# Kernel optimization log

Measured on AMD Instinct MI355X. Metric: run time of the kernel, lower is better.

## Reference

```python
import jax, jax.numpy as jnp
import numpy as np


def _iir_forward(b_coeff, rho, psi, u_in, y_init, u_init):
    # Coefficient computation: stable 2nd-order resonator parameterization
    r = jax.nn.sigmoid(rho)
    theta = jnp.pi * jax.nn.sigmoid(psi)
    a1 = -2.0 * r * jnp.cos(theta)
    a2 = r * r

    B, T = u_in.shape
    nb = b_coeff.shape[0]  # number of FIR taps (n_b)

    # FIR (moving-average) part, fully vectorized over batch and time:
    # v[t] = sum_k b[k] * u[t-k]; past inputs come from u_init = [u[-1], u[-2], ...]
    u_ext = jnp.concatenate([u_init[:, ::-1], u_in], axis=1)  # [B, T + nb - 1], time-ordered
    v = jnp.zeros_like(u_in)
    for k in range(nb):  # small fixed loop over filter taps
        v = v + b_coeff[k] * jax.lax.dynamic_slice_in_dim(u_ext, nb - 1 - k, T, axis=1)

    # AR (recursive) part: y[t] = v[t] - a1*y[t-1] - a2*y[t-2]  (sequential scan over time)
    def step(carry, v_t):
        y1, y2 = carry  # y[t-1], y[t-2], each [B]
        y = v_t - a1 * y1 - a2 * y2
        return (y, y1), y

    init = (y_init[:, 0], y_init[:, 1])  # [y[-1], y[-2]] per lfiltic convention
    _, y = jax.lax.scan(step, init, v.T)  # y: [T, B]
    return y.T  # [B, T]


def setup_inputs() -> dict:
    key = jax.random.key(0)
    k1, k2, k3, k4 = jax.random.split(key, 4)
    B, T, NB = 1024, 16384, 3
    return {
        "b_coeff": 0.1 * jax.random.normal(k1, (NB,), dtype=jnp.float32),
        "rho": jnp.asarray(jax.random.normal(k2, (), dtype=jnp.float32) + 0.9),
        "psi": jnp.asarray(jax.random.normal(k3, (), dtype=jnp.float32) * 0.5),
        "u_in": jax.random.normal(k4, (B, T), dtype=jnp.float32),
        "y_init": jnp.zeros((B, 2), dtype=jnp.float32),
        "u_init": jnp.zeros((B, NB - 1), dtype=jnp.float32),
    }


def reference(b_coeff, rho, psi, u_in, y_init, u_init):
    return _iir_forward(b_coeff, rho, psi, u_in, y_init, u_init)
```

## Files before the change

kernel.cpp:

```cpp
#include <hip/hip_runtime.h>
#include <math.h>


#define TLEN  16384
#define HALF  8192
#define NT    256
#define CK    32
#define NCH   256
#define SCAN_OFF  HALF
#define CARRY_OFF (SCAN_OFF + 2*NCH)
#define LDS_FLOATS (CARRY_OFF + 2)

__device__ __forceinline__ int swz(int s) { return s ^ ((s >> 3) & 7); }

__device__ __forceinline__ void mat2_sq(float& m00, float& m01, float& m10, float& m11) {
    float t00 = m00*m00 + m01*m10;
    float t01 = m00*m01 + m01*m11;
    float t10 = m10*m00 + m11*m10;
    float t11 = m10*m01 + m11*m11;
    m00 = t00; m01 = t01; m10 = t10; m11 = t11;
}

__device__ __forceinline__ void bar_lgkm() {
    asm volatile("s_waitcnt lgkmcnt(0)" ::: "memory");
    __builtin_amdgcn_s_barrier();
    __builtin_amdgcn_sched_barrier(0);
}

__global__ __launch_bounds__(NT, 4)
void iir_kernel(const float* __restrict__ bc,
                const float* __restrict__ rho_p,
                const float* __restrict__ psi_p,
                const float* __restrict__ u_in,
                const float* __restrict__ y_init,
                const float* __restrict__ u_init,
                float* __restrict__ y_out)
{
    __shared__ float lds[LDS_FLOATS];
    float4* lds4 = (float4*)lds;
    const int row = blockIdx.x;
    const int tid = threadIdx.x;

    const float* urow = u_in  + (size_t)row * TLEN;
    float*       orow = y_out + (size_t)row * TLEN;
    const float4* up  = (const float4*)urow;

    float4 uv[8];
    #pragma unroll
    for (int k = 0; k < 8; ++k) uv[k] = up[tid + k * NT];
    float hm2, hm1;
    if (tid == 0) {
        hm2 = u_init[2*row + 1];
        hm1 = u_init[2*row + 0];
    } else {
        float2 hh = *(const float2*)(urow + CK*tid - 2);
        hm2 = hh.x; hm1 = hh.y;
    }

    const float rho = rho_p[0];
    const float psi = psi_p[0];
    const float r   = 1.0f / (1.0f + expf(-rho));
    const float th  = 3.14159265358979323846f / (1.0f + expf(-psi));
    const float a1  = -2.0f * r * cosf(th);
    const float a2  = r * r;
    const float b0  = bc[0], b1 = bc[1], b2 = bc[2];

    const int xr = tid & 7;
    float v[CK];

    #pragma unroll
    for (int h = 0; h < 2; ++h) {
        #pragma unroll
        for (int k = 0; k < 8; ++k) {
            int g = tid + k * NT;
            lds4[swz(g)] = uv[k];
        }
        bar_lgkm();

        float4 u4[8];
        #pragma unroll
        for (int j = 0; j < 8; ++j) u4[j] = lds4[8*tid + (j ^ xr)];

        float um2 = hm2, um1 = hm1;
        float y1 = 0.0f, y2 = 0.0f;
        #define STEP(UC, IDX) {                                        \
            float uc_ = (UC);                                          \
            float vv_ = fmaf(b2, um2, fmaf(b1, um1, b0 * uc_));        \
            v[IDX] = vv_;                                              \
            float y_ = fmaf(-a1, y1, fmaf(-a2, y2, vv_));              \
            y2 = y1; y1 = y_;                                          \
            um2 = um1; um1 = uc_; }
        #pragma unroll
        for (int q = 0; q < 8; ++q) {
            STEP(u4[q].x, 4*q + 0);
            STEP(u4[q].y, 4*q + 1);
            STEP(u4[q].z, 4*q + 2);
            STEP(u4[q].w, 4*q + 3);
        }
        #undef STEP

        *(float2*)&lds[SCAN_OFF + 2*tid] = make_float2(y1, y2);

        if (h == 0) {
            #pragma unroll
            for (int k = 0; k < 8; ++k) uv[k] = up[(HALF/4) + tid + k * NT];
            float2 hh = *(const float2*)(urow + HALF + CK*tid - 2);
            hm2 = hh.x; hm1 = hh.y;
        }

        bar_lgkm();

        if (tid < 64) {
            const int l = tid;
            float m00 = -a1, m01 = -a2, m10 = 1.0f, m11 = 0.0f;
            #pragma unroll
            for (int s = 0; s < 5; ++s) mat2_sq(m00, m01, m10, m11);

            float4 q0 = *(const float4*)&lds[SCAN_OFF + 8*l];
            float4 q1 = *(const float4*)&lds[SCAN_OFF + 8*l + 4];
            float da[4] = {q0.x, q0.z, q1.x, q1.z};
            float db[4] = {q0.y, q0.w, q1.y, q1.w};

            float seed0 = 0.0f, seed1 = 0.0f;
            if (l == 0) {
                if (h == 0) { seed0 = y_init[2*row]; seed1 = y_init[2*row + 1]; }
                else        { seed0 = lds[CARRY_OFF]; seed1 = lds[CARRY_OFF + 1]; }
            }
            float s0 = seed0, s1 = seed1;
            #pragma unroll
            for (int m = 0; m < 4; ++m) {
                float n0 = fmaf(m00, s0, fmaf(m01, s1, da[m]));
                float n1 = fmaf(m10, s0, fmaf(m11, s1, db[m]));
                s0 = n0; s1 = n1;
            }
            float w00 = m00, w01 = m01, w10 = m10, w11 = m11;
            mat2_sq(w00, w01, w10, w11);
            mat2_sq(w00, w01, w10, w11);
            #pragma unroll
            for (int p = 0; p < 6; ++p) {
                float o0 = __shfl_up(s0, 1 << p);
                float o1 = __shfl_up(s1, 1 << p);
                if (l >= (1 << p)) {
                    s0 = fmaf(w00, o0, fmaf(w01, o1, s0));
                    s1 = fmaf(w10, o0, fmaf(w11, o1, s1));
                }
                if (p < 5) mat2_sq(w00, w01, w10, w11);
            }
            float p0 = __shfl_up(s0, 1);
            float p1 = __shfl_up(s1, 1);
            if (l == 0) { p0 = seed0; p1 = seed1; }
            float c0 = p0, c1 = p1;
            #pragma unroll
            for (int m = 0; m < 4; ++m) {
                *(float2*)&lds[SCAN_OFF + 2*(4*l + m)] = make_float2(c0, c1);
                float n0 = fmaf(m00, c0, fmaf(m01, c1, da[m]));
                float n1 = fmaf(m10, c0, fmaf(m11, c1, db[m]));
                c0 = n0; c1 = n1;
            }
            if (l == 63 && h == 0) {
                lds[CARRY_OFF]     = c0;
                lds[CARRY_OFF + 1] = c1;
            }
        }
        bar_lgkm();

        float2 inc = *(const float2*)&lds[SCAN_OFF + 2*tid];
        float y1f = inc.x, y2f = inc.y;
        #pragma unroll
        for (int q = 0; q < 8; ++q) {
            float ya = fmaf(-a1, y1f, fmaf(-a2, y2f, v[4*q + 0]));
            float yb = fmaf(-a1, ya,  fmaf(-a2, y1f, v[4*q + 1]));
            float yc = fmaf(-a1, yb,  fmaf(-a2, ya,  v[4*q + 2]));
            float yd = fmaf(-a1, yc,  fmaf(-a2, yb,  v[4*q + 3]));
            float4 w; w.x = ya; w.y = yb; w.z = yc; w.w = yd;
            lds4[8*tid + (q ^ xr)] = w;
            y2f = yc; y1f = yd;
        }
        bar_lgkm();

        float4* op = (float4*)(orow + h * HALF);
        #pragma unroll
        for (int k = 0; k < 8; ++k) {
            int g = tid + k * NT;
            op[g] = lds4[swz(g)];
        }
        if (h == 0) bar_lgkm();
    }
}

extern "C" void kernel_launch(void* const* d_in, const int* in_sizes, int n_in,
                              void* d_out, int out_size, void* d_ws, size_t ws_size,
                              hipStream_t stream) {
    const float* bc    = (const float*)d_in[0];
    const float* rho   = (const float*)d_in[1];
    const float* psi   = (const float*)d_in[2];
    const float* u_in  = (const float*)d_in[3];
    const float* y_in  = (const float*)d_in[4];
    const float* u_ini = (const float*)d_in[5];
    float* y = (float*)d_out;
    const int B = in_sizes[3] / TLEN;
    iir_kernel<<<B, NT, 0, stream>>>(bc, rho, psi, u_in, y_in, u_ini, y);
}
```

Baseline: 143.9 us.

## Load input directly into LDS via global_load_lds and overlap second-half fetch

Replaces the register-staged global loads plus LDS stores with direct global-to-LDS loads (global_load_lds), with the swizzle applied on the global address side. The second-half input fetch is issued after the first half's outputs are read into registers, so it overlaps the output stores, and a vmcnt wait gates it. Halo values now come from LDS instead of extra global loads, with a carry slot for the cross-half boundary. This removes the VGPR round-trip and extra LDS write pass, at the cost of more delicate vmcnt and barrier ordering.

```diff
diff --git a/kernel.cpp b/kernel.cpp
--- a/kernel.cpp
+++ b/kernel.cpp
@@ -7,11 +7,20 @@
 #define NT    256
 #define CK    32
 #define NCH   256
-#define SCAN_OFF  HALF
+#define NSLOT (HALF/4)
+#define SCAN_OFF  8192
 #define CARRY_OFF (SCAN_OFF + 2*NCH)
-#define LDS_FLOATS (CARRY_OFF + 2)
+#define UH_OFF    (CARRY_OFF + 2)
+#define LDS_FLOATS (UH_OFF + 2)
 
 __device__ __forceinline__ int swz(int s) { return s ^ ((s >> 3) & 7); }
+
+__device__ __forceinline__ void gll16(const float4* g, float4* l) {
+    __builtin_amdgcn_global_load_lds(
+        (const __attribute__((address_space(1))) unsigned int*)g,
+        (__attribute__((address_space(3))) unsigned int*)l,
+        16, 0, 0);
+}
 
 __device__ __forceinline__ void mat2_sq(float& m00, float& m01, float& m10, float& m11) {
     float t00 = m00*m00 + m01*m10;
@@ -40,23 +49,20 @@
     float4* lds4 = (float4*)lds;
     const int row = blockIdx.x;
     const int tid = threadIdx.x;
-
-    const float* urow = u_in  + (size_t)row * TLEN;
-    float*       orow = y_out + (size_t)row * TLEN;
-    const float4* up  = (const float4*)urow;
-
-    float4 uv[8];
+    const int xr  = tid & 7;
+
+    const float*  urow = u_in  + (size_t)row * TLEN;
+    float*        orow = y_out + (size_t)row * TLEN;
+    const float4* up   = (const float4*)urow;
+
     #pragma unroll
-    for (int k = 0; k < 8; ++k) uv[k] = up[tid + k * NT];
-    float hm2, hm1;
-    if (tid == 0) {
-        hm2 = u_init[2*row + 1];
-        hm1 = u_init[2*row + 0];
-    } else {
-        float2 hh = *(const float2*)(urow + CK*tid - 2);
-        hm2 = hh.x; hm1 = hh.y;
+    for (int k = 0; k < 8; ++k) {
+        int p = k * NT + tid;
+        gll16(up + swz(p), lds4 + p);
     }
-
+    __builtin_amdgcn_sched_barrier(0);
+
+    float2 ui = *(const float2*)&u_init[2*row];
     const float rho = rho_p[0];
     const float psi = psi_p[0];
     const float r   = 1.0f / (1.0f + expf(-rho));
@@ -65,23 +71,28 @@
     const float a2  = r * r;
     const float b0  = bc[0], b1 = bc[1], b2 = bc[2];
 
-    const int xr = tid & 7;
     float v[CK];
 
     #pragma unroll
     for (int h = 0; h < 2; ++h) {
-        #pragma unroll
-        for (int k = 0; k < 8; ++k) {
-            int g = tid + k * NT;
-            lds4[swz(g)] = uv[k];
-        }
-        bar_lgkm();
-
+        if (h == 0) asm volatile("s_waitcnt vmcnt(0)" ::: "memory");
+        else        asm volatile("s_waitcnt vmcnt(8)" ::: "memory");
+        __builtin_amdgcn_s_barrier();
+        __builtin_amdgcn_sched_barrier(0);
+
+        float um2, um1;
+        if (tid == 0) {
+            if (h == 0) { um2 = ui.y; um1 = ui.x; }
+            else        { um2 = lds[UH_OFF]; um1 = lds[UH_OFF + 1]; }
+        } else {
+            int hq = swz(8*tid - 1);
+            float2 hh = *(const float2*)&lds[4*hq + 2];
+            um2 = hh.x; um1 = hh.y;
+        }
         float4 u4[8];
         #pragma unroll
         for (int j = 0; j < 8; ++j) u4[j] = lds4[8*tid + (j ^ xr)];
 
-        float um2 = hm2, um1 = hm1;
         float y1 = 0.0f, y2 = 0.0f;
         #define STEP(UC, IDX) {                                        \
             float uc_ = (UC);                                          \
@@ -100,14 +111,10 @@
         #undef STEP
 
         *(float2*)&lds[SCAN_OFF + 2*tid] = make_float2(y1, y2);
-
-        if (h == 0) {
-            #pragma unroll
-            for (int k = 0; k < 8; ++k) uv[k] = up[(HALF/4) + tid + k * NT];
-            float2 hh = *(const float2*)(urow + HALF + CK*tid - 2);
-            hm2 = hh.x; hm1 = hh.y;
-        }
-
+        if (h == 0 && tid == NT - 1) {
+            lds[UH_OFF]     = um2;
+            lds[UH_OFF + 1] = um1;
+        }
         bar_lgkm();
 
         if (tid < 64) {
@@ -178,13 +185,26 @@
         }
         bar_lgkm();
 
+        float4 yreg[8];
+        #pragma unroll
+        for (int k = 0; k < 8; ++k) yreg[k] = lds4[swz(k * NT + tid)];
+        asm volatile("s_waitcnt lgkmcnt(0)" ::: "memory");
+
+        if (h == 0) {
+            __builtin_amdgcn_s_barrier();
+            __builtin_amdgcn_sched_barrier(0);
+            #pragma unroll
+            for (int k = 0; k < 8; ++k) {
+                int p = k * NT + tid;
+                gll16(up + (HALF/4) + swz(p), lds4 + p);
+            }
+            __builtin_amdgcn_sched_barrier(0);
+        }
+
         float4* op = (float4*)(orow + h * HALF);
         #pragma unroll
-        for (int k = 0; k < 8; ++k) {
-            int g = tid + k * NT;
-            op[g] = lds4[swz(g)];
-        }
-        if (h == 0) bar_lgkm();
+        for (int k = 0; k < 8; ++k) op[k * NT + tid] = yreg[k];
+        __builtin_amdgcn_sched_barrier(0);
     }
 }
 
```

Measured after the change: 146.9 us. 1.02x slower.
